# Kernel optimization log

Hardware: AMD Instinct MI355X
Metric: run time of the kernel (lower is better)

## Reference

```python
import jax, jax.numpy as jnp
import numpy as np

# dims (see shape_source)
N = 20000      # spots / graph nodes
G = 3000       # genes
NF = 256       # NFeature = CrossAttention dim
D_IN = 256     # dims_spot[0]
HID = 64       # dims_spot[1]
OUT = 16       # dims_spot[2]
H = 3          # GATv2 heads
E1 = 640000
E2 = 320000
SLOPE = 0.2    # leaky relu negative slope (GATv2 + CrossAttention alpha)


def _gat_params(key, din, hid, heads):
    k = jax.random.split(key, 3)
    s = 1.0 / np.sqrt(din)
    Wl = jax.random.normal(k[0], (din, heads * hid), jnp.float32) * s
    Wr = jax.random.normal(k[1], (din, heads * hid), jnp.float32) * s
    att = jax.random.normal(k[2], (heads, hid), jnp.float32) * s
    bl = jnp.zeros((heads * hid,), jnp.float32)
    br = jnp.zeros((heads * hid,), jnp.float32)
    b = jnp.zeros((hid,), jnp.float32)
    return Wl, bl, Wr, br, att, b


def setup_inputs() -> dict:
    key = jax.random.key(0)
    ks = jax.random.split(key, 16)
    inp = {
        "gene_freq_mtx": jax.random.normal(ks[0], (NF, G), jnp.float32),
        "gene_eigvecs_T": jax.random.normal(ks[1], (G, N), jnp.float32) / np.sqrt(G),
        "spot_freq_mtx": jax.random.normal(ks[2], (N, D_IN), jnp.float32),
        "spot_eigvecs_T": jax.random.normal(ks[3], (D_IN, NF), jnp.float32) / np.sqrt(D_IN),
        "spotnet": jax.random.randint(ks[4], (2, E1), 0, N, jnp.int32),
        "spotnet_cluster": jax.random.randint(ks[5], (2, E2), 0, N, jnp.int32),
    }
    for name, din, kk in [("c1", D_IN, ks[6]), ("c1p", D_IN, ks[7]), ("c3", OUT, ks[8]), ("c3p", OUT, ks[9])]:
        Wl, bl, Wr, br, att, b = _gat_params(kk, din, HID, H)
        inp[name + "_Wl"] = Wl; inp[name + "_bl"] = bl
        inp[name + "_Wr"] = Wr; inp[name + "_br"] = br
        inp[name + "_att"] = att; inp[name + "_b"] = b
    inp["W2"] = jax.random.normal(ks[10], (2 * HID, OUT), jnp.float32) / np.sqrt(2 * HID)
    inp["b2"] = jnp.zeros((OUT,), jnp.float32)
    inp["W4"] = jax.random.normal(ks[11], (2 * HID, D_IN), jnp.float32) / np.sqrt(2 * HID)
    inp["b4"] = jnp.zeros((D_IN,), jnp.float32)
    inp["a1"] = jax.random.normal(ks[12], (2 * NF, 1), jnp.float32) * 0.05
    inp["a2"] = jax.random.normal(ks[13], (2 * NF, 1), jnp.float32) * 0.05
    return inp


def gatv2(x, edge_index, Wl, bl, Wr, br, att, b, n):
    """PyG GATv2Conv, concat=False (head mean), add_self_loops=False, eval mode."""
    heads, c = att.shape
    src, dst = edge_index[0], edge_index[1]
    xl = (x @ Wl + bl).reshape(-1, heads, c)   # source transform [N,H,C]
    xr = (x @ Wr + br).reshape(-1, heads, c)   # target transform [N,H,C]
    m = jax.nn.leaky_relu(xl[src] + xr[dst], SLOPE)          # [E,H,C]
    e = jnp.einsum('ehc,hc->eh', m, att)                      # [E,H]
    emax = jax.ops.segment_max(e, dst, num_segments=n)        # [N,H]
    emax = jnp.where(jnp.isfinite(emax), emax, 0.0)           # empty segments
    p = jnp.exp(e - emax[dst])
    denom = jax.ops.segment_sum(p, dst, num_segments=n)       # [N,H]
    alpha = p / jnp.maximum(denom, 1e-16)[dst]                # segment softmax
    out = jax.ops.segment_sum(alpha[:, :, None] * xl[src], dst, num_segments=n)
    return out.mean(axis=1) + b                                # [N,C]


def reference(gene_freq_mtx, gene_eigvecs_T, spot_freq_mtx, spot_eigvecs_T,
              c1_Wl, c1_bl, c1_Wr, c1_br, c1_att, c1_b,
              c1p_Wl, c1p_bl, c1p_Wr, c1p_br, c1p_att, c1p_b,
              W2, b2,
              c3_Wl, c3_bl, c3_Wr, c3_br, c3_att, c3_b,
              c3p_Wl, c3p_bl, c3p_Wr, c3p_br, c3p_att, c3p_b,
              W4, b4, a1, a2, spotnet, spotnet_cluster):
    n = spot_freq_mtx.shape[0]
    # GAT (cluster=True)
    h1n = gatv2(spot_freq_mtx, spotnet, c1_Wl, c1_bl, c1_Wr, c1_br, c1_att, c1_b, n)
    h1p = gatv2(spot_freq_mtx, spotnet_cluster, c1p_Wl, c1p_bl, c1p_Wr, c1p_br, c1p_att, c1p_b, n)
    h1 = jax.nn.elu(jnp.concatenate([h1n, h1p], axis=1))
    h2 = h1 @ W2 + b2                                          # emb_spot [N,OUT]
    h3n = gatv2(h2, spotnet, c3_Wl, c3_bl, c3_Wr, c3_br, c3_att, c3_b, n)
    h3p = gatv2(h2, spotnet_cluster, c3p_Wl, c3p_bl, c3p_Wr, c3p_br, c3p_att, c3p_b, n)
    h3 = jax.nn.elu(jnp.concatenate([h3n, h3p], axis=1))
    h4 = h3 @ W4 + b4                                          # mtx_res_spot [N,D_IN]
    # iGFT + clip-at-zero (== relu)
    Xg = jax.nn.relu(gene_eigvecs_T.T @ gene_freq_mtx.T)       # [N,NF]
    Xs = jax.nn.relu(h4 @ spot_eigvecs_T)                      # [N,NF]
    # CrossAttention (dropout=0.0)
    cat = jnp.concatenate([Xg, Xs], axis=1)                    # [N,2NF]
    e = jax.nn.leaky_relu(jnp.concatenate([cat @ a1, cat @ a2], axis=1), SLOPE)
    lam = jax.nn.softmax(e, axis=1)                            # [N,2]
    res = lam[:, :1] * Xg + lam[:, 1:] * Xs
    return (res, lam, h2, h4)
```

## Files before the change

### kernel.cpp

```cpp
#include <hip/hip_runtime.h>

typedef unsigned short u16;
typedef __attribute__((ext_vector_type(8))) short bf16x8;
typedef __attribute__((ext_vector_type(4))) float floatx4;

#define NSPOT 20000
#define NGENE 3000
#define E1N   640000
#define E2N   320000

#define OFF_RES 0
#define OFF_LAM 5120000
#define OFF_H2  5160000
#define OFF_H4  5480000

__device__ __forceinline__ float b2f(u16 u){
  union { unsigned int i; float f; } v; v.i = ((unsigned int)u) << 16; return v.f;
}
__device__ __forceinline__ u16 f2b(float f){
  union { float f; unsigned int i; } v; v.f = f;
  unsigned int i = v.i;
  return (u16)((i + 0x7FFFu + ((i >> 16) & 1u)) >> 16);
}
__device__ __forceinline__ void stout(void* O, size_t i, float v, int isbf){
  if (isbf) ((u16*)O)[i] = f2b(v); else ((float*)O)[i] = v;
}
__device__ __forceinline__ u16 ldu(const void* p, size_t i, int isbf){
  return isbf ? ((const u16*)p)[i] : f2b(((const float*)p)[i]);
}

__global__ void sniff_kernel(const u16* __restrict__ x, int* __restrict__ flag){
  int lane = threadIdx.x;
  u16 u = x[lane * 2];
  int e = (u >> 7) & 0xFF;
  int sane = (u == 0) || (e >= 0x60 && e <= 0xA0);
  unsigned long long b = __ballot(sane);
  if (lane == 0) flag[0] = (__popcll(b) >= 48) ? 1 : 0;
}

struct ConvSeg { const void* src; u16* dst; int n; };
struct ConvBatch { ConvSeg s[14]; };
__global__ void convbatch_kernel(ConvBatch cb, const int* __restrict__ dflag){
  ConvSeg S = cb.s[blockIdx.y];
  int i = blockIdx.x * 256 + threadIdx.x;
  if (i < S.n) S.dst[i] = ldu(S.src, i, dflag[0]);
}

__global__ void conv3_kernel(const void* __restrict__ s0, u16* __restrict__ d0, int n0,
                             const void* __restrict__ s1, u16* __restrict__ d1, int n1,
                             const void* __restrict__ s2, u16* __restrict__ d2, int n2,
                             const int* __restrict__ dflag){
  int i = blockIdx.x * 256 + threadIdx.x;
  const void* src; u16* dst; int local;
  if (i < n0){ src = s0; dst = d0; local = i; }
  else if (i < n0 + n1){ src = s1; dst = d1; local = i - n0; }
  else if (i < n0 + n1 + n2){ src = s2; dst = d2; local = i - n0 - n1; }
  else return;
  size_t b = (size_t)local * 4;
  u16 o[4];
  if (dflag[0]){
    *(uint2*)o = *(const uint2*)((const u16*)src + b);
  } else {
    float4 f = *(const float4*)((const float*)src + b);
    o[0]=f2b(f.x); o[1]=f2b(f.y); o[2]=f2b(f.z); o[3]=f2b(f.w);
  }
  *(uint2*)(dst + b) = *(uint2*)o;
}

__global__ void hist2_kernel(const int* __restrict__ dst0, int E0, int* __restrict__ cnt0,
                             const int* __restrict__ dst1, int E1, int* __restrict__ cnt1){
  const int* dst = blockIdx.y ? dst1 : dst0;
  int* cnt = blockIdx.y ? cnt1 : cnt0;
  int E = blockIdx.y ? E1 : E0;
  int e = blockIdx.x * 256 + threadIdx.x;
  if (e < E){ int d = dst[e]; if ((unsigned)d < (unsigned)NSPOT) atomicAdd(&cnt[d], 1); }
}

__global__ void scan2_kernel(const int* __restrict__ c0, int* __restrict__ o0, int* __restrict__ u0,
                             const int* __restrict__ c1, int* __restrict__ o1, int* __restrict__ u1,
                             int n){
  const int* cnt = blockIdx.x ? c1 : c0;
  int* off = blockIdx.x ? o1 : o0;
  int* cur = blockIdx.x ? u1 : u0;
  __shared__ int part[256];
  int tid = threadIdx.x;
  int chunk = (n + 255) / 256;
  int lo = tid * chunk; if (lo > n) lo = n;
  int hi = lo + chunk; if (hi > n) hi = n;
  int s = 0;
  for (int i = lo; i < hi; i++) s += cnt[i];
  part[tid] = s;
  __syncthreads();
  if (tid == 0){
    int run = 0;
    for (int i = 0; i < 256; i++){ int t = part[i]; part[i] = run; run += t; }
  }
  __syncthreads();
  int run = part[tid];
  for (int i = lo; i < hi; i++){ off[i] = run; cur[i] = run; run += cnt[i]; }
  if (hi == n) off[n] = run;
}

__global__ void scatter2_kernel(const int* __restrict__ src0, const int* __restrict__ dst0,
                                int* __restrict__ cur0, int* __restrict__ out0, int E0,
                                const int* __restrict__ src1, const int* __restrict__ dst1,
                                int* __restrict__ cur1, int* __restrict__ out1, int E1){
  const int* src = blockIdx.y ? src1 : src0;
  const int* dst = blockIdx.y ? dst1 : dst0;
  int* cur = blockIdx.y ? cur1 : cur0;
  int* out = blockIdx.y ? out1 : out0;
  int E = blockIdx.y ? E1 : E0;
  int e = blockIdx.x * 256 + threadIdx.x;
  if (e < E){
    int d = dst[e];
    if ((unsigned)d < (unsigned)NSPOT){
      int p = atomicAdd(&cur[d], 1);
      if ((unsigned)p < (unsigned)E) out[p] = src[e];
    }
  }
}

struct AsmSet {
  const void *Wl, *bl, *Wr, *br, *Wlp, *blp, *Wrp, *brp;
  u16* Wcat; u16* bcat; int Kdim;
};
__global__ void assemble2_kernel(AsmSet s0, AsmSet s1, const int* __restrict__ dflag){
  AsmSet S = blockIdx.y ? s1 : s0;
  int isbf = dflag[0];
  int idx = blockIdx.x * 256 + threadIdx.x;
  int total = S.Kdim * 768;
  if (idx < total){
    int k = idx / 768, j = idx % 768;
    int seg = j / 192, jj = j % 192;
    const void* W = (seg == 0) ? S.Wl : (seg == 1) ? S.Wr : (seg == 2) ? S.Wlp : S.Wrp;
    S.Wcat[idx] = ldu(W, (size_t)k * 192 + jj, isbf);
  }
  if (idx < 768){
    int seg = idx / 192, jj = idx % 192;
    const void* b = (seg == 0) ? S.bl : (seg == 1) ? S.br : (seg == 2) ? S.blp : S.brp;
    S.bcat[idx] = ldu(b, jj, isbf);
  }
}

template<int BMI, bool A_KM, bool B_NK, bool A_EXT, bool B_EXT, bool RELU, bool HAS_BIAS, bool C_OUT, bool C2, bool C_F32>
__global__ __launch_bounds__(256) void gemm_mfma(
    const void* __restrict__ A, const void* __restrict__ B,
    const u16* __restrict__ bias, void* __restrict__ Cp, u16* __restrict__ Cp2,
    const int* __restrict__ dflag, size_t aoff, size_t coff,
    int M, int N, int K, int kchunk, size_t cstride,
    int lda, int ldb, int ldc, int ldc2)
{
  const int isbf = dflag[0];
  constexpr int BM = 64 * BMI, BK = 32, LDA = BK + 8, LDB = BK + 8;
  __shared__ __align__(16) u16 As[BM * LDA];
  __shared__ __align__(16) u16 Bs[64 * LDB];
  const u16*   A16 = (const u16*)A + aoff;
  const float* A32 = (const float*)A + aoff;
  const u16*   B16 = (const u16*)B;
  const float* B32 = (const float*)B;
  auto ldA = [&](size_t i) -> u16 { return (!A_EXT || isbf) ? A16[i] : f2b(A32[i]); };
  auto ldB = [&](size_t i) -> u16 { return (!B_EXT || isbf) ? B16[i] : f2b(B32[i]); };

  int tid = threadIdx.x;
  int lane = tid & 63, w = tid >> 6;
  int m0 = blockIdx.y * BM, n0 = blockIdx.x * 64;
  int kbeg = (int)blockIdx.z * kchunk;
  int kend = (K < kbeg + kchunk) ? K : (kbeg + kchunk);
  floatx4 acc[BMI][4] = {};
  int quad = lane >> 4;
  int nk = (kend - kbeg + BK - 1) / BK;
  for (int kt = 0; kt < nk; kt++){
    int k0 = kbeg + kt * BK;
    if (!A_KM){
#pragma unroll
      for (int i = 0; i < BMI; i++){
        int id = tid + i * 256;
        int r = id >> 2, c = (id & 3) * 8;
        int gm = m0 + r, gk = k0 + c;
        if (gm < M && gk + 8 <= K){
          if (!A_EXT || isbf){
            *(uint4*)&As[r * LDA + c] = *(const uint4*)(A16 + (size_t)gm * lda + gk);
          } else {
            const float* p = A32 + (size_t)gm * lda + gk;
            float4 f0 = *(const float4*)p, f1 = *(const float4*)(p + 4);
            u16* d = &As[r * LDA + c];
            d[0]=f2b(f0.x); d[1]=f2b(f0.y); d[2]=f2b(f0.z); d[3]=f2b(f0.w);
            d[4]=f2b(f1.x); d[5]=f2b(f1.y); d[6]=f2b(f1.z); d[7]=f2b(f1.w);
          }
        } else {
          for (int e = 0; e < 8; e++)
            As[r * LDA + c + e] = (gm < M && gk + e < K) ? ldA((size_t)gm * lda + gk + e) : (u16)0;
        }
      }
    } else {
#pragma unroll
      for (int i = 0; i < BMI; i++){
        int id = tid + i * 256;
        int kk, rr;
        if (BMI == 2){ kk = id >> 4; rr = (id & 15) * 8; }
        else         { kk = id >> 3; rr = (id & 7) * 8; }
        int gk = k0 + kk, gm = m0 + rr;
        if (gk < K && gm + 8 <= M){
          if (!A_EXT || isbf){
            uint4 v = *(const uint4*)(A16 + (size_t)gk * lda + gm);
            const u16* pv = (const u16*)&v;
#pragma unroll
            for (int e = 0; e < 8; e++) As[(rr + e) * LDA + kk] = pv[e];
          } else {
            const float* p = A32 + (size_t)gk * lda + gm;
            float4 f0 = *(const float4*)p, f1 = *(const float4*)(p + 4);
            As[(rr+0)*LDA+kk]=f2b(f0.x); As[(rr+1)*LDA+kk]=f2b(f0.y);
            As[(rr+2)*LDA+kk]=f2b(f0.z); As[(rr+3)*LDA+kk]=f2b(f0.w);
            As[(rr+4)*LDA+kk]=f2b(f1.x); As[(rr+5)*LDA+kk]=f2b(f1.y);
            As[(rr+6)*LDA+kk]=f2b(f1.z); As[(rr+7)*LDA+kk]=f2b(f1.w);
          }
        } else {
          for (int e = 0; e < 8; e++)
            As[(rr + e) * LDA + kk] = (gk < K && gm + e < M) ? ldA((size_t)gk * lda + gm + e) : (u16)0;
        }
      }
    }
    if (B_NK){
      int r = tid >> 2, c = (tid & 3) * 8;
      int gn = n0 + r, gk = k0 + c;
      if (gn < N && gk + 8 <= K){
        if (!B_EXT || isbf){
          *(uint4*)&Bs[r * LDB + c] = *(const uint4*)(B16 + (size_t)gn * ldb + gk);
        } else {
          const float* p = B32 + (size_t)gn * ldb + gk;
          float4 f0 = *(const float4*)p, f1 = *(const float4*)(p + 4);
          u16* d = &Bs[r * LDB + c];
          d[0]=f2b(f0.x); d[1]=f2b(f0.y); d[2]=f2b(f0.z); d[3]=f2b(f0.w);
          d[4]=f2b(f1.x); d[5]=f2b(f1.y); d[6]=f2b(f1.z); d[7]=f2b(f1.w);
        }
      } else {
        for (int e = 0; e < 8; e++)
          Bs[r * LDB + c + e] = (gn < N && gk + e < K) ? ldB((size_t)gn * ldb + gk + e) : (u16)0;
      }
    } else {
      int kk = tid >> 3, nn = (tid & 7) * 8;
      int gk = k0 + kk, gn = n0 + nn;
      if (gk < K && gn + 8 <= N){
        if (!B_EXT || isbf){
          uint4 v = *(const uint4*)(B16 + (size_t)gk * ldb + gn);
          const u16* pv = (const u16*)&v;
#pragma unroll
          for (int e = 0; e < 8; e++) Bs[(nn + e) * LDB + kk] = pv[e];
        } else {
          const float* p = B32 + (size_t)gk * ldb + gn;
          float4 f0 = *(const float4*)p, f1 = *(const float4*)(p + 4);
          Bs[(nn+0)*LDB+kk]=f2b(f0.x); Bs[(nn+1)*LDB+kk]=f2b(f0.y);
          Bs[(nn+2)*LDB+kk]=f2b(f0.z); Bs[(nn+3)*LDB+kk]=f2b(f0.w);
          Bs[(nn+4)*LDB+kk]=f2b(f1.x); Bs[(nn+5)*LDB+kk]=f2b(f1.y);
          Bs[(nn+6)*LDB+kk]=f2b(f1.z); Bs[(nn+7)*LDB+kk]=f2b(f1.w);
        }
      } else {
        for (int e = 0; e < 8; e++)
          Bs[(nn + e) * LDB + kk] = (gk < K && gn + e < N) ? ldB((size_t)gk * ldb + gn + e) : (u16)0;
      }
    }
    __syncthreads();
    bf16x8 af[BMI];
#pragma unroll
    for (int mi = 0; mi < BMI; mi++)
      af[mi] = *(const bf16x8*)&As[(w * (16 * BMI) + mi * 16 + (lane & 15)) * LDA + quad * 8];
#pragma unroll
    for (int ni = 0; ni < 4; ni++){
      bf16x8 bfr = *(const bf16x8*)&Bs[(ni * 16 + (lane & 15)) * LDB + quad * 8];
#pragma unroll
      for (int mi = 0; mi < BMI; mi++)
        acc[mi][ni] = __builtin_amdgcn_mfma_f32_16x16x32_bf16(af[mi], bfr, acc[mi][ni], 0, 0, 0);
    }
    __syncthreads();
  }
#pragma unroll
  for (int mi = 0; mi < BMI; mi++)
#pragma unroll
    for (int ni = 0; ni < 4; ni++)
#pragma unroll
      for (int r = 0; r < 4; r++){
        int row = m0 + w * (16 * BMI) + mi * 16 + quad * 4 + r;
        int col = n0 + ni * 16 + (lane & 15);
        if (row < M && col < N){
          float v = acc[mi][ni][r];
          if (HAS_BIAS) v += b2f(bias[col]);
          if (RELU) v = fmaxf(v, 0.f);
          size_t ci = coff + (size_t)blockIdx.z * cstride + (size_t)row * ldc + col;
          if (C_F32) ((float*)Cp)[ci] = v;
          else if (!C_OUT) ((u16*)Cp)[ci] = f2b(v);
          else stout(Cp, ci, v, isbf);
          if (C2) Cp2[(size_t)row * ldc2 + col] = f2b(v);
        }
      }
}

__global__ __launch_bounds__(256) void redtr_kernel(const float* __restrict__ P,
                                                    u16* __restrict__ XG){
  __shared__ float tile[64 * 65];
  int s0 = blockIdx.x * 64;
  int c0 = blockIdx.y * 64;
  int t = threadIdx.x;
#pragma unroll
  for (int i = 0; i < 4; i++){
    int c = i * 16 + (t >> 4);
    int sp = (t & 15) * 4;
    int gs = s0 + sp;
    size_t base = (size_t)(c0 + c) * NSPOT + gs;
    float v0 = 0.f, v1 = 0.f, v2 = 0.f, v3 = 0.f;
    if (gs + 4 <= NSPOT){
      float4 a = *(const float4*)(P + base);
      float4 b = *(const float4*)(P + (size_t)256 * NSPOT + base);
      v0 = a.x + b.x; v1 = a.y + b.y; v2 = a.z + b.z; v3 = a.w + b.w;
    } else {
      for (int e = 0; e < 4; e++){
        if (gs + e < NSPOT){
          float x = P[base + e] + P[(size_t)256 * NSPOT + base + e];
          if (e == 0) v0 = x; else if (e == 1) v1 = x; else if (e == 2) v2 = x; else v3 = x;
        }
      }
    }
    tile[c * 65 + sp + 0] = fmaxf(v0, 0.f);
    tile[c * 65 + sp + 1] = fmaxf(v1, 0.f);
    tile[c * 65 + sp + 2] = fmaxf(v2, 0.f);
    tile[c * 65 + sp + 3] = fmaxf(v3, 0.f);
  }
  __syncthreads();
#pragma unroll
  for (int i = 0; i < 2; i++){
    int sp = i * 32 + (t >> 3);
    int cc = (t & 7) * 8;
    int gs = s0 + sp;
    if (gs < NSPOT){
      u16 o[8];
#pragma unroll
      for (int e = 0; e < 8; e++) o[e] = f2b(tile[(cc + e) * 65 + sp]);
      *(uint4*)&XG[(size_t)gs * 256 + c0 + cc] = *(uint4*)o;
    }
  }
}

struct GatSet {
  const int* off; const int* srcs; const u16* att; const u16* bias;
  int xl_off, xr_off, out_off, E;
};
__global__ __launch_bounds__(256) void gat2_kernel(
    const u16* __restrict__ Y, GatSet SA, GatSet SB,
    u16* __restrict__ aggout, int n)
{
  int half = gridDim.x >> 1;
  int selB = (int)blockIdx.x >= half;
  GatSet S = selB ? SB : SA;
  int bx = blockIdx.x - (selB ? half : 0);
  int wid = (bx * 256 + threadIdx.x) >> 6;
  int lane = threadIdx.x & 63;
  if (wid >= n) return;
  int sub = lane >> 3;
  int cbase = (lane & 7) * 8;
  const int ldY = 768;
  size_t drow = (size_t)wid * ldY;

  float xr[3][8], at[3][8];
#pragma unroll
  for (int h = 0; h < 3; h++){
    uint4 vx = *(const uint4*)(Y + drow + S.xr_off + h * 64 + cbase);
    uint4 va = *(const uint4*)(S.att + h * 64 + cbase);
    const u16* px = (const u16*)&vx;
    const u16* pa = (const u16*)&va;
#pragma unroll
    for (int j = 0; j < 8; j++){ xr[h][j] = b2f(px[j]); at[h][j] = b2f(pa[j]); }
  }

  int beg = S.off[wid], end = S.off[wid + 1];
  beg = max(0, min(beg, S.E));
  end = max(beg, min(end, S.E));

  float mh[3] = {-INFINITY, -INFINITY, -INFINITY};
  float lh[3] = {0.f, 0.f, 0.f};
  float ac[3][8] = {};

  uint4 xa[3] = {};
  int s_b = 0;
  if (beg < end){
    int e0 = beg + sub;
    int s = (e0 < end) ? S.srcs[e0] : 0;
    if ((unsigned)s >= (unsigned)NSPOT) s = 0;
    const u16* p = Y + (size_t)s * ldY + S.xl_off + cbase;
#pragma unroll
    for (int h = 0; h < 3; h++) xa[h] = *(const uint4*)(p + h * 64);
    if (beg + 8 < end){
      int e1 = beg + 8 + sub;
      int s1 = (e1 < end) ? S.srcs[e1] : 0;
      if ((unsigned)s1 >= (unsigned)NSPOT) s1 = 0;
      s_b = s1;
    }
  }

  for (int b = beg; b < end; b += 8){
    uint4 xc[3];
#pragma unroll
    for (int h = 0; h < 3; h++) xc[h] = xa[h];
    bool act = (b + sub) < end;

    if (b + 8 < end){
      const u16* p = Y + (size_t)s_b * ldY + S.xl_off + cbase;
#pragma unroll
      for (int h = 0; h < 3; h++) xa[h] = *(const uint4*)(p + h * 64);
      if (b + 16 < end){
        int e2 = b + 16 + sub;
        int s2 = (e2 < end) ? S.srcs[e2] : 0;
        if ((unsigned)s2 >= (unsigned)NSPOT) s2 = 0;
        s_b = s2;
      }
    }

    float xl[3][8];
    float t0 = 0.f, t1 = 0.f, t2 = 0.f;
    {
      const u16* p0 = (const u16*)&xc[0];
      const u16* p1 = (const u16*)&xc[1];
      const u16* p2 = (const u16*)&xc[2];
#pragma unroll
      for (int j = 0; j < 8; j++){
        float x0 = b2f(p0[j]); xl[0][j] = x0;
        float u0 = x0 + xr[0][j]; u0 = fmaxf(u0, 0.2f * u0);
        t0 = __builtin_fmaf(at[0][j], u0, t0);
        float x1 = b2f(p1[j]); xl[1][j] = x1;
        float u1 = x1 + xr[1][j]; u1 = fmaxf(u1, 0.2f * u1);
        t1 = __builtin_fmaf(at[1][j], u1, t1);
        float x2 = b2f(p2[j]); xl[2][j] = x2;
        float u2 = x2 + xr[2][j]; u2 = fmaxf(u2, 0.2f * u2);
        t2 = __builtin_fmaf(at[2][j], u2, t2);
      }
    }
#pragma unroll
    for (int d = 1; d < 8; d <<= 1){
      t0 += __shfl_xor(t0, d, 64);
      t1 += __shfl_xor(t1, d, 64);
      t2 += __shfl_xor(t2, d, 64);
    }
    if (act){
      float tt[3] = {t0, t1, t2};
#pragma unroll
      for (int h = 0; h < 3; h++){
        float nm = fmaxf(mh[h], tt[h]);
        if (nm > mh[h]){
          float sc = __expf(mh[h] - nm);
          lh[h] *= sc;
#pragma unroll
          for (int j = 0; j < 8; j++) ac[h][j] *= sc;
          mh[h] = nm;
        }
        float w = __expf(tt[h] - mh[h]);
        lh[h] += w;
#pragma unroll
        for (int j = 0; j < 8; j++) ac[h][j] = __builtin_fmaf(w, xl[h][j], ac[h][j]);
      }
    }
  }

  float o[8] = {};
#pragma unroll
  for (int h = 0; h < 3; h++){
    float gm = fmaxf(mh[h], __shfl_xor(mh[h], 8, 64));
    gm = fmaxf(gm, __shfl_xor(gm, 16, 64));
    gm = fmaxf(gm, __shfl_xor(gm, 32, 64));
    float sc = (mh[h] == -INFINITY) ? 0.f : __expf(mh[h] - gm);
    float L = lh[h] * sc;
    L += __shfl_xor(L, 8, 64);
    L += __shfl_xor(L, 16, 64);
    L += __shfl_xor(L, 32, 64);
    float inv = 1.f / fmaxf(L, 1e-16f);
#pragma unroll
    for (int j = 0; j < 8; j++){
      float a = ac[h][j] * sc;
      a += __shfl_xor(a, 8, 64);
      a += __shfl_xor(a, 16, 64);
      a += __shfl_xor(a, 32, 64);
      o[j] += a * inv;
    }
  }
  if (sub == 0){
    u16 ov[8];
#pragma unroll
    for (int j = 0; j < 8; j++){
      float v = o[j] * (1.f / 3.f) + b2f(S.bias[cbase + j]);
      v = (v > 0.f) ? v : expm1f(v);
      if (!(fabsf(v) < 1e30f)) v = 0.f;
      ov[j] = f2b(v);
    }
    *(uint4*)&aggout[(size_t)wid * 128 + S.out_off + cbase] = *(uint4*)ov;
  }
}

__global__ __launch_bounds__(256) void h2y2_kernel(
    const u16* __restrict__ AGG, const u16* __restrict__ W2, const u16* __restrict__ b2,
    const u16* __restrict__ Wcat2, const u16* __restrict__ bcat2,
    void* __restrict__ OUT, u16* __restrict__ Y2,
    const int* __restrict__ dflag, int n){
  __shared__ float w2s[128 * 16];
  __shared__ float as_[16][128];
  __shared__ float h[16][16];
  __shared__ __align__(16) u16 ws_[16 * 768];
  int isbf = dflag[0];
  int tid = threadIdx.x;
  for (int i = tid; i < 128 * 16; i += 256) w2s[i] = b2f(W2[i]);
  for (int i = tid; i < 1536; i += 256) ((uint4*)ws_)[i] = ((const uint4*)Wcat2)[i];
  int m0 = blockIdx.x * 16;
  for (int i = tid; i < 16 * 128; i += 256){
    int r = i >> 7, c = i & 127; int m = m0 + r;
    as_[r][c] = (m < n) ? b2f(AGG[(size_t)m * 128 + c]) : 0.f;
  }
  __syncthreads();
  {
    int r = tid >> 4, j = tid & 15;
    int m = m0 + r;
    float acc = b2f(b2[j]);
    for (int k = 0; k < 128; k++) acc += as_[r][k] * w2s[k * 16 + j];
    h[r][j] = acc;
    if (m < n) stout(OUT, (size_t)OFF_H2 + (size_t)m * 16 + j, acc, isbf);
  }
  __syncthreads();
  int j = tid;
  float acc[16][3];
  float bj0 = b2f(bcat2[j]), bj1 = b2f(bcat2[j + 256]), bj2 = b2f(bcat2[j + 512]);
#pragma unroll
  for (int r = 0; r < 16; r++){ acc[r][0] = bj0; acc[r][1] = bj1; acc[r][2] = bj2; }
  for (int k = 0; k < 16; k++){
    float w0 = b2f(ws_[k * 768 + j]);
    float w1 = b2f(ws_[k * 768 + j + 256]);
    float w2 = b2f(ws_[k * 768 + j + 512]);
#pragma unroll
    for (int r = 0; r < 16; r++){
      float hv = h[r][k];
      acc[r][0] += hv * w0; acc[r][1] += hv * w1; acc[r][2] += hv * w2;
    }
  }
#pragma unroll
  for (int r = 0; r < 16; r++){
    int m = m0 + r;
    if (m < n){
      size_t base = (size_t)m * 768;
      Y2[base + j] = f2b(acc[r][0]);
      Y2[base + j + 256] = f2b(acc[r][1]);
      Y2[base + j + 512] = f2b(acc[r][2]);
    }
  }
}

__global__ __launch_bounds__(256) void cross_attn_kernel(
    const u16* __restrict__ XG, const u16* __restrict__ XS,
    const u16* __restrict__ a1, const u16* __restrict__ a2,
    void* __restrict__ OUT, const int* __restrict__ dflag, int n){
  int wid = (blockIdx.x * 256 + threadIdx.x) >> 6;
  int lane = threadIdx.x & 63;
  if (wid >= n) return;
  int isbf = dflag[0];
  int c0 = lane * 4;
  size_t base = (size_t)wid * 256 + c0;
  float g[4], s[4];
#pragma unroll
  for (int e = 0; e < 4; e++){ g[e] = b2f(XG[base + e]); s[e] = b2f(XS[base + e]); }
  float p1 = 0.f, p2 = 0.f;
#pragma unroll
  for (int e = 0; e < 4; e++){
    p1 += g[e] * b2f(a1[c0 + e]) + s[e] * b2f(a1[256 + c0 + e]);
    p2 += g[e] * b2f(a2[c0 + e]) + s[e] * b2f(a2[256 + c0 + e]);
  }
#pragma unroll
  for (int d = 32; d > 0; d >>= 1){
    p1 += __shfl_xor(p1, d, 64);
    p2 += __shfl_xor(p2, d, 64);
  }
  float e1 = (p1 > 0.f) ? p1 : 0.2f * p1;
  float e2 = (p2 > 0.f) ? p2 : 0.2f * p2;
  float mx = fmaxf(e1, e2);
  float w1 = __expf(e1 - mx), w2 = __expf(e2 - mx);
  float inv = 1.f / (w1 + w2);
  float l0 = w1 * inv, l1 = w2 * inv;
#pragma unroll
  for (int e = 0; e < 4; e++)
    stout(OUT, (size_t)OFF_RES + base + e, l0 * g[e] + l1 * s[e], isbf);
  if (lane == 0){
    stout(OUT, (size_t)OFF_LAM + (size_t)wid * 2,     l0, isbf);
    stout(OUT, (size_t)OFF_LAM + (size_t)wid * 2 + 1, l1, isbf);
  }
}

extern "C" void kernel_launch(void* const* d_in, const int* in_sizes, int n_in,
                              void* d_out, int out_size, void* d_ws, size_t ws_size,
                              hipStream_t stream) {
  const void* gene_freq = d_in[0];
  const void* gene_eig  = d_in[1];
  const void* spot_freq = d_in[2];
  const void* spot_eig  = d_in[3];
  const int* net1 = (const int*)d_in[4];
  const int* net2 = (const int*)d_in[5];
  const void *c1_Wl=d_in[6],  *c1_bl=d_in[7],  *c1_Wr=d_in[8],  *c1_br=d_in[9],  *c1_att=d_in[10], *c1_b=d_in[11];
  const void *c1p_Wl=d_in[12],*c1p_bl=d_in[13],*c1p_Wr=d_in[14],*c1p_br=d_in[15],*c1p_att=d_in[16],*c1p_b=d_in[17];
  const void *c3_Wl=d_in[18], *c3_bl=d_in[19], *c3_Wr=d_in[20], *c3_br=d_in[21], *c3_att=d_in[22], *c3_b=d_in[23];
  const void *c3p_Wl=d_in[24],*c3p_bl=d_in[25],*c3p_Wr=d_in[26],*c3p_br=d_in[27],*c3p_att=d_in[28],*c3p_b=d_in[29];
  const void *W2=d_in[30], *b2=d_in[31], *W4=d_in[32], *b4=d_in[33], *a1=d_in[34], *a2=d_in[35];

  char* p0 = (char*)d_ws;
  char* p = p0;
  auto carve = [&](size_t bytes) -> char* {
    char* r = p; p += (bytes + 255) & ~(size_t)255; return r;
  };
  int*   flag  = (int*) carve(256);
  int*   cnt1  = (int*) carve((NSPOT + 2) * 4);
  int*   off1  = (int*) carve((NSPOT + 2) * 4);
  int*   cur1  = (int*) carve((NSPOT + 2) * 4);
  int*   srcs1 = (int*) carve((size_t)E1N * 4);
  int*   cnt2  = (int*) carve((NSPOT + 2) * 4);
  int*   off2  = (int*) carve((NSPOT + 2) * 4);
  int*   cur2  = (int*) carve((NSPOT + 2) * 4);
  int*   srcs2 = (int*) carve((size_t)E2N * 4);
  u16*   Wcat1 = (u16*) carve(256 * 768 * 2);
  u16*   bcat1 = (u16*) carve(2048);
  u16*   Wcat2 = (u16*) carve(16 * 768 * 2);
  u16*   bcat2 = (u16*) carve(2048);
  u16*   attc1  = (u16*)carve(192 * 2);
  u16*   attc1p = (u16*)carve(192 * 2);
  u16*   attc3  = (u16*)carve(192 * 2);
  u16*   attc3p = (u16*)carve(192 * 2);
  u16*   bc1  = (u16*)carve(64 * 2);
  u16*   bc1p = (u16*)carve(64 * 2);
  u16*   bc3  = (u16*)carve(64 * 2);
  u16*   bc3p = (u16*)carve(64 * 2);
  u16*   W2c  = (u16*)carve(2048 * 2);
  u16*   b2c  = (u16*)carve(16 * 2);
  u16*   W4c  = (u16*)carve(32768 * 2);
  u16*   b4c  = (u16*)carve(256 * 2);
  u16*   a1c  = (u16*)carve(512 * 2);
  u16*   a2c  = (u16*)carve(512 * 2);
  u16*   GF16 = (u16*) carve((size_t)256 * 3000 * 2);
  u16*   SE16 = (u16*) carve((size_t)256 * 256 * 2);
  u16*   SF16 = (u16*) carve((size_t)NSPOT * 256 * 2);
  u16*   H4B  = (u16*) carve((size_t)NSPOT * 256 * 2);
  u16*   AGG  = (u16*) carve((size_t)NSPOT * 128 * 2);
  u16*   XG   = (u16*) carve((size_t)NSPOT * 256 * 2);
  char*  R    = carve((size_t)2 * 256 * NSPOT * 4);
  float* Pbuf = (float*)R;
  u16*   Y    = (u16*)R;
  u16*   XS   = (u16*)(R + (size_t)NSPOT * 768 * 2);

  sniff_kernel<<<1, 64, 0, stream>>>((const u16*)spot_freq, flag);
  hipMemsetAsync(cnt1, 0, NSPOT * 4, stream);
  hipMemsetAsync(cnt2, 0, NSPOT * 4, stream);
  hist2_kernel<<<dim3((E1N + 255) / 256, 2), 256, 0, stream>>>(
      net1 + E1N, E1N, cnt1, net2 + E2N, E2N, cnt2);
  scan2_kernel<<<2, 256, 0, stream>>>(cnt1, off1, cur1, cnt2, off2, cur2, NSPOT);
  scatter2_kernel<<<dim3((E1N + 255) / 256, 2), 256, 0, stream>>>(
      net1, net1 + E1N, cur1, srcs1, E1N, net2, net2 + E2N, cur2, srcs2, E2N);

  ConvBatch cb;
  cb.s[0]  = {c1_att,  attc1,  192}; cb.s[1]  = {c1p_att, attc1p, 192};
  cb.s[2]  = {c3_att,  attc3,  192}; cb.s[3]  = {c3p_att, attc3p, 192};
  cb.s[4]  = {c1_b, bc1, 64}; cb.s[5]  = {c1p_b, bc1p, 64};
  cb.s[6]  = {c3_b, bc3, 64}; cb.s[7]  = {c3p_b, bc3p, 64};
  cb.s[8]  = {W2, W2c, 2048}; cb.s[9]  = {b2, b2c, 16};
  cb.s[10] = {W4, W4c, 32768}; cb.s[11] = {b4, b4c, 256};
  cb.s[12] = {a1, a1c, 512}; cb.s[13] = {a2, a2c, 512};
  convbatch_kernel<<<dim3(128, 14), 256, 0, stream>>>(cb, flag);

  {
    int n0 = 256 * 3000 / 4, n1 = 256 * 256 / 4, n2 = NSPOT * 256 / 4;
    int tot = n0 + n1 + n2;
    conv3_kernel<<<(tot + 255) / 256, 256, 0, stream>>>(
        gene_freq, GF16, n0, spot_eig, SE16, n1, spot_freq, SF16, n2, flag);
  }

  AsmSet as0 = {c1_Wl, c1_bl, c1_Wr, c1_br, c1p_Wl, c1p_bl, c1p_Wr, c1p_br, Wcat1, bcat1, 256};
  AsmSet as1 = {c3_Wl, c3_bl, c3_Wr, c3_br, c3p_Wl, c3p_bl, c3p_Wr, c3p_br, Wcat2, bcat2, 16};
  assemble2_kernel<<<dim3((256 * 768 + 255) / 256, 2), 256, 0, stream>>>(as0, as1, flag);

  GatSet g1a = {off1, srcs1, attc1,  bc1,  0,   192, 0,  E1N};
  GatSet g1b = {off2, srcs2, attc1p, bc1p, 384, 576, 64, E2N};
  GatSet g3a = {off1, srcs1, attc3,  bc3,  0,   192, 0,  E1N};
  GatSet g3b = {off2, srcs2, attc3p, bc3p, 384, 576, 64, E2N};

  gemm_mfma<2, false, false, false, true, false, false, false, false, true>
      <<<dim3(313, 2, 2), 256, 0, stream>>>(
      GF16, gene_eig, nullptr, Pbuf, nullptr, flag, 0, 0,
      256, NSPOT, NGENE, 1504, (size_t)256 * NSPOT, NGENE, NSPOT, NSPOT, 0);
  redtr_kernel<<<dim3(313, 4), 256, 0, stream>>>(Pbuf, XG);

  gemm_mfma<2, false, false, false, false, false, true, false, false, false>
      <<<dim3(12, 157), 256, 0, stream>>>(
      SF16, Wcat1, bcat1, Y, nullptr, flag, 0, 0,
      NSPOT, 768, 256, 256, 0, 256, 768, 768, 0);
  gat2_kernel<<<10000, 256, 0, stream>>>(Y, g1a, g1b, AGG, NSPOT);
  h2y2_kernel<<<1250, 256, 0, stream>>>(AGG, W2c, b2c, Wcat2, bcat2, d_out, Y, flag, NSPOT);
  gat2_kernel<<<10000, 256, 0, stream>>>(Y, g3a, g3b, AGG, NSPOT);
  gemm_mfma<1, false, false, false, false, false, true, true, true, false>
      <<<dim3(4, 313), 256, 0, stream>>>(
      AGG, W4c, b4c, d_out, H4B, flag, 0, OFF_H4,
      NSPOT, 256, 128, 128, 0, 128, 256, 256, 256);
  gemm_mfma<1, false, false, false, false, true, false, false, false, false>
      <<<dim3(4, 313), 256, 0, stream>>>(
      H4B, SE16, nullptr, XS, nullptr, flag, 0, 0,
      NSPOT, 256, 256, 256, 0, 256, 256, 256, 0);
  cross_attn_kernel<<<5000, 256, 0, stream>>>(XG, XS, a1c, a2c, d_out, flag, NSPOT);

  (void)in_sizes; (void)n_in; (void)out_size; (void)ws_size;
}
```

Before: 1.024 ms.

## Replace split-K gene GEMM and reduce-transpose with a fused XG kernel

Swaps the split-K gemm (written as fp32 partials) plus the separate reduce/transpose/relu kernel for one kernel that computes the whole 256xN XG output per 64-spot block. Each block stages gene_freq chunks in LDS and reads gene_eigvecs columns straight from global memory, applying relu and writing bf16 rows directly. This drops the fp32 partial buffer round-trip and one launch. The cost is lower parallelism: 313 blocks with 64 accumulator registers per thread, each block reloading all of GF and doing strided scalar global loads of GE.

```diff
diff --git a/kernel.cpp b/kernel.cpp
--- a/kernel.cpp
+++ b/kernel.cpp
@@ -142,13 +142,79 @@
   }
 }
 
-template<int BMI, bool A_KM, bool B_NK, bool A_EXT, bool B_EXT, bool RELU, bool HAS_BIAS, bool C_OUT, bool C2, bool C_F32>
+__global__ __launch_bounds__(256) void xg_kernel(
+    const u16* __restrict__ GF,
+    const void* __restrict__ GE,
+    u16* __restrict__ XG,
+    const int* __restrict__ dflag)
+{
+  constexpr int KC = 128;
+  constexpr int LDA = KC + 8;
+  __shared__ __align__(16) u16 As[256 * LDA];
+  const int isbf = dflag[0];
+  const float* GE32 = (const float*)GE;
+  const u16*   GE16 = (const u16*)GE;
+  int tid = threadIdx.x;
+  int lane = tid & 63, w = tid >> 6;
+  int quad = lane >> 4, c16 = lane & 15;
+  int n = blockIdx.x * 64 + w * 16 + c16;
+  int nc = min(n, NSPOT - 1);
+  floatx4 acc[16] = {};
+  const int NCH = (NGENE + KC - 1) / KC;
+  for (int ch = 0; ch < NCH; ch++){
+    int k0 = ch * KC;
+    {
+      const u16* src = GF + (size_t)tid * NGENE + k0;
+      u16* dst = &As[tid * LDA];
+#pragma unroll
+      for (int i = 0; i < KC / 8; i++){
+        if (k0 + i * 8 + 8 <= NGENE){
+          *(uint4*)(dst + i * 8) = *(const uint4*)(src + i * 8);
+        } else {
+          for (int e = 0; e < 8; e++)
+            dst[i * 8 + e] = (k0 + i * 8 + e < NGENE) ? src[i * 8 + e] : (u16)0;
+        }
+      }
+    }
+    __syncthreads();
+#pragma unroll
+    for (int s = 0; s < KC / 32; s++){
+      u16 bfr[8];
+#pragma unroll
+      for (int j = 0; j < 8; j++){
+        int k = k0 + s * 32 + quad * 8 + j;
+        int kcl = min(k, NGENE - 1);
+        float bv = isbf ? b2f(GE16[(size_t)kcl * NSPOT + nc])
+                        : GE32[(size_t)kcl * NSPOT + nc];
+        bfr[j] = f2b(bv);
+      }
+      bf16x8 bv8 = *(bf16x8*)bfr;
+#pragma unroll
+      for (int mt = 0; mt < 16; mt++){
+        bf16x8 av = *(const bf16x8*)&As[(mt * 16 + c16) * LDA + s * 32 + quad * 8];
+        acc[mt] = __builtin_amdgcn_mfma_f32_16x16x32_bf16(av, bv8, acc[mt], 0, 0, 0);
+      }
+    }
+    __syncthreads();
+  }
+  if (n < NSPOT){
+    u16* row = XG + (size_t)n * 256;
+#pragma unroll
+    for (int mt = 0; mt < 16; mt++){
+      u16 o[4];
+#pragma unroll
+      for (int r = 0; r < 4; r++) o[r] = f2b(fmaxf(acc[mt][r], 0.f));
+      *(uint2*)(row + mt * 16 + quad * 4) = *(uint2*)o;
+    }
+  }
+}
+
+template<int BMI, bool A_KM, bool B_NK, bool A_EXT, bool B_EXT, bool RELU, bool HAS_BIAS, bool C_OUT, bool C2>
 __global__ __launch_bounds__(256) void gemm_mfma(
     const void* __restrict__ A, const void* __restrict__ B,
     const u16* __restrict__ bias, void* __restrict__ Cp, u16* __restrict__ Cp2,
     const int* __restrict__ dflag, size_t aoff, size_t coff,
-    int M, int N, int K, int kchunk, size_t cstride,
-    int lda, int ldb, int ldc, int ldc2)
+    int M, int N, int K, int lda, int ldb, int ldc, int ldc2)
 {
   const int isbf = dflag[0];
   constexpr int BM = 64 * BMI, BK = 32, LDA = BK + 8, LDB = BK + 8;
@@ -164,13 +230,11 @@
   int tid = threadIdx.x;
   int lane = tid & 63, w = tid >> 6;
   int m0 = blockIdx.y * BM, n0 = blockIdx.x * 64;
-  int kbeg = (int)blockIdx.z * kchunk;
-  int kend = (K < kbeg + kchunk) ? K : (kbeg + kchunk);
   floatx4 acc[BMI][4] = {};
   int quad = lane >> 4;
-  int nk = (kend - kbeg + BK - 1) / BK;
+  int nk = (K + BK - 1) / BK;
   for (int kt = 0; kt < nk; kt++){
-    int k0 = kbeg + kt * BK;
+    int k0 = kt * BK;
     if (!A_KM){
 #pragma unroll
       for (int i = 0; i < BMI; i++){
@@ -285,58 +349,12 @@
           float v = acc[mi][ni][r];
           if (HAS_BIAS) v += b2f(bias[col]);
           if (RELU) v = fmaxf(v, 0.f);
-          size_t ci = coff + (size_t)blockIdx.z * cstride + (size_t)row * ldc + col;
-          if (C_F32) ((float*)Cp)[ci] = v;
-          else if (!C_OUT) ((u16*)Cp)[ci] = f2b(v);
+          size_t ci = coff + (size_t)row * ldc + col;
+          if (!C_OUT) ((u16*)Cp)[ci] = f2b(v);
           else stout(Cp, ci, v, isbf);
           if (C2) Cp2[(size_t)row * ldc2 + col] = f2b(v);
         }
       }
-}
-
-__global__ __launch_bounds__(256) void redtr_kernel(const float* __restrict__ P,
-                                                    u16* __restrict__ XG){
-  __shared__ float tile[64 * 65];
-  int s0 = blockIdx.x * 64;
-  int c0 = blockIdx.y * 64;
-  int t = threadIdx.x;
-#pragma unroll
-  for (int i = 0; i < 4; i++){
-    int c = i * 16 + (t >> 4);
-    int sp = (t & 15) * 4;
-    int gs = s0 + sp;
-    size_t base = (size_t)(c0 + c) * NSPOT + gs;
-    float v0 = 0.f, v1 = 0.f, v2 = 0.f, v3 = 0.f;
-    if (gs + 4 <= NSPOT){
-      float4 a = *(const float4*)(P + base);
-      float4 b = *(const float4*)(P + (size_t)256 * NSPOT + base);
-      v0 = a.x + b.x; v1 = a.y + b.y; v2 = a.z + b.z; v3 = a.w + b.w;
-    } else {
-      for (int e = 0; e < 4; e++){
-        if (gs + e < NSPOT){
-          float x = P[base + e] + P[(size_t)256 * NSPOT + base + e];
-          if (e == 0) v0 = x; else if (e == 1) v1 = x; else if (e == 2) v2 = x; else v3 = x;
-        }
-      }
-    }
-    tile[c * 65 + sp + 0] = fmaxf(v0, 0.f);
-    tile[c * 65 + sp + 1] = fmaxf(v1, 0.f);
-    tile[c * 65 + sp + 2] = fmaxf(v2, 0.f);
-    tile[c * 65 + sp + 3] = fmaxf(v3, 0.f);
-  }
-  __syncthreads();
-#pragma unroll
-  for (int i = 0; i < 2; i++){
-    int sp = i * 32 + (t >> 3);
-    int cc = (t & 7) * 8;
-    int gs = s0 + sp;
-    if (gs < NSPOT){
-      u16 o[8];
-#pragma unroll
-      for (int e = 0; e < 8; e++) o[e] = f2b(tile[(cc + e) * 65 + sp]);
-      *(uint4*)&XG[(size_t)gs * 256 + c0 + cc] = *(uint4*)o;
-    }
-  }
 }
 
 struct GatSet {
@@ -640,7 +658,6 @@
   u16*   AGG  = (u16*) carve((size_t)NSPOT * 128 * 2);
   u16*   XG   = (u16*) carve((size_t)NSPOT * 256 * 2);
   char*  R    = carve((size_t)2 * 256 * NSPOT * 4);
-  float* Pbuf = (float*)R;
   u16*   Y    = (u16*)R;
   u16*   XS   = (u16*)(R + (size_t)NSPOT * 768 * 2);
 
@@ -679,27 +696,23 @@
   GatSet g3a = {off1, srcs1, attc3,  bc3,  0,   192, 0,  E1N};
   GatSet g3b = {off2, srcs2, attc3p, bc3p, 384, 576, 64, E2N};
 
-  gemm_mfma<2, false, false, false, true, false, false, false, false, true>
-      <<<dim3(313, 2, 2), 256, 0, stream>>>(
-      GF16, gene_eig, nullptr, Pbuf, nullptr, flag, 0, 0,
-      256, NSPOT, NGENE, 1504, (size_t)256 * NSPOT, NGENE, NSPOT, NSPOT, 0);
-  redtr_kernel<<<dim3(313, 4), 256, 0, stream>>>(Pbuf, XG);
-
-  gemm_mfma<2, false, false, false, false, false, true, false, false, false>
+  xg_kernel<<<313, 256, 0, stream>>>(GF16, gene_eig, XG, flag);
+
+  gemm_mfma<2, false, false, false, false, false, true, false, false>
       <<<dim3(12, 157), 256, 0, stream>>>(
       SF16, Wcat1, bcat1, Y, nullptr, flag, 0, 0,
-      NSPOT, 768, 256, 256, 0, 256, 768, 768, 0);
+      NSPOT, 768, 256, 256, 768, 768, 0);
   gat2_kernel<<<10000, 256, 0, stream>>>(Y, g1a, g1b, AGG, NSPOT);
   h2y2_kernel<<<1250, 256, 0, stream>>>(AGG, W2c, b2c, Wcat2, bcat2, d_out, Y, flag, NSPOT);
   gat2_kernel<<<10000, 256, 0, stream>>>(Y, g3a, g3b, AGG, NSPOT);
-  gemm_mfma<1, false, false, false, false, false, true, true, true, false>
+  gemm_mfma<1, false, false, false, false, false, true, true, true>
       <<<dim3(4, 313), 256, 0, stream>>>(
       AGG, W4c, b4c, d_out, H4B, flag, 0, OFF_H4,
-      NSPOT, 256, 128, 128, 0, 128, 256, 256, 256);
-  gemm_mfma<1, false, false, false, false, true, false, false, false, false>
+      NSPOT, 256, 128, 128, 256, 256, 256);
+  gemm_mfma<1, false, false, false, false, true, false, false, false>
       <<<dim3(4, 313), 256, 0, stream>>>(
       H4B, SE16, nullptr, XS, nullptr, flag, 0, 0,
-      NSPOT, 256, 256, 256, 0, 256, 256, 256, 0);
+      NSPOT, 256, 256, 256, 256, 256, 0);
   cross_attn_kernel<<<5000, 256, 0, stream>>>(XG, XS, a1c, a2c, d_out, flag, NSPOT);
 
   (void)in_sizes; (void)n_in; (void)out_size; (void)ws_size;
```

Result: slower. 1.102 ms (+7.6%).

## Write gene GEMM partials transposed and split K four ways with simpler reduction

Applied to the files above, without the earlier changes.

The gene-frequency GEMM now writes its fp32 split-K partials directly in spot-major (transposed) layout using float4 stores, so the follow-up kernel becomes a plain elementwise sum, relu and bf16 convert with no shared-memory transpose. The GEMM tile grows to BM=256 (covering all 256 rows in one block), and the K split goes from 2 to 4 chunks of 768. This removes the separate transpose pass and raises parallelism over K. In exchange the partial buffer doubles in size, and the reduction kernel reads four fp32 planes. The transposed float4 stores are strided by column, which may hurt write coalescing.

```diff
diff --git a/kernel.cpp b/kernel.cpp
--- a/kernel.cpp
+++ b/kernel.cpp
@@ -142,7 +142,7 @@
   }
 }
 
-template<int BMI, bool A_KM, bool B_NK, bool A_EXT, bool B_EXT, bool RELU, bool HAS_BIAS, bool C_OUT, bool C2, bool C_F32>
+template<int BMI, bool A_KM, bool B_NK, bool A_EXT, bool B_EXT, bool RELU, bool HAS_BIAS, bool C_OUT, bool C2, bool C_F32TR>
 __global__ __launch_bounds__(256) void gemm_mfma(
     const void* __restrict__ A, const void* __restrict__ B,
     const u16* __restrict__ bias, void* __restrict__ Cp, u16* __restrict__ Cp2,
@@ -273,6 +273,23 @@
     }
     __syncthreads();
   }
+  if (C_F32TR){
+#pragma unroll
+    for (int mi = 0; mi < BMI; mi++)
+#pragma unroll
+      for (int ni = 0; ni < 4; ni++){
+        int rowb = m0 + w * (16 * BMI) + mi * 16 + quad * 4;
+        int col = n0 + ni * 16 + (lane & 15);
+        if (col < N && rowb + 4 <= M){
+          float4 o;
+          o.x = acc[mi][ni][0]; o.y = acc[mi][ni][1];
+          o.z = acc[mi][ni][2]; o.w = acc[mi][ni][3];
+          *(float4*)((float*)Cp + coff + (size_t)blockIdx.z * cstride
+                     + (size_t)col * ldc + rowb) = o;
+        }
+      }
+    return;
+  }
 #pragma unroll
   for (int mi = 0; mi < BMI; mi++)
 #pragma unroll
@@ -285,58 +302,29 @@
           float v = acc[mi][ni][r];
           if (HAS_BIAS) v += b2f(bias[col]);
           if (RELU) v = fmaxf(v, 0.f);
-          size_t ci = coff + (size_t)blockIdx.z * cstride + (size_t)row * ldc + col;
-          if (C_F32) ((float*)Cp)[ci] = v;
-          else if (!C_OUT) ((u16*)Cp)[ci] = f2b(v);
+          size_t ci = coff + (size_t)row * ldc + col;
+          if (!C_OUT) ((u16*)Cp)[ci] = f2b(v);
           else stout(Cp, ci, v, isbf);
           if (C2) Cp2[(size_t)row * ldc2 + col] = f2b(v);
         }
       }
 }
 
-__global__ __launch_bounds__(256) void redtr_kernel(const float* __restrict__ P,
+__global__ __launch_bounds__(256) void xgred_kernel(const float* __restrict__ P,
                                                     u16* __restrict__ XG){
-  __shared__ float tile[64 * 65];
-  int s0 = blockIdx.x * 64;
-  int c0 = blockIdx.y * 64;
-  int t = threadIdx.x;
-#pragma unroll
-  for (int i = 0; i < 4; i++){
-    int c = i * 16 + (t >> 4);
-    int sp = (t & 15) * 4;
-    int gs = s0 + sp;
-    size_t base = (size_t)(c0 + c) * NSPOT + gs;
-    float v0 = 0.f, v1 = 0.f, v2 = 0.f, v3 = 0.f;
-    if (gs + 4 <= NSPOT){
-      float4 a = *(const float4*)(P + base);
-      float4 b = *(const float4*)(P + (size_t)256 * NSPOT + base);
-      v0 = a.x + b.x; v1 = a.y + b.y; v2 = a.z + b.z; v3 = a.w + b.w;
-    } else {
-      for (int e = 0; e < 4; e++){
-        if (gs + e < NSPOT){
-          float x = P[base + e] + P[(size_t)256 * NSPOT + base + e];
-          if (e == 0) v0 = x; else if (e == 1) v1 = x; else if (e == 2) v2 = x; else v3 = x;
-        }
-      }
-    }
-    tile[c * 65 + sp + 0] = fmaxf(v0, 0.f);
-    tile[c * 65 + sp + 1] = fmaxf(v1, 0.f);
-    tile[c * 65 + sp + 2] = fmaxf(v2, 0.f);
-    tile[c * 65 + sp + 3] = fmaxf(v3, 0.f);
-  }
-  __syncthreads();
-#pragma unroll
-  for (int i = 0; i < 2; i++){
-    int sp = i * 32 + (t >> 3);
-    int cc = (t & 7) * 8;
-    int gs = s0 + sp;
-    if (gs < NSPOT){
-      u16 o[8];
-#pragma unroll
-      for (int e = 0; e < 8; e++) o[e] = f2b(tile[(cc + e) * 65 + sp]);
-      *(uint4*)&XG[(size_t)gs * 256 + c0 + cc] = *(uint4*)o;
-    }
-  }
+  size_t i = ((size_t)blockIdx.x * 256 + threadIdx.x) * 4;
+  const size_t ZS = (size_t)NSPOT * 256;
+  if (i >= ZS) return;
+  float4 a = *(const float4*)(P + i);
+  float4 b = *(const float4*)(P + ZS + i);
+  float4 c = *(const float4*)(P + 2 * ZS + i);
+  float4 d = *(const float4*)(P + 3 * ZS + i);
+  u16 o[4];
+  o[0] = f2b(fmaxf(a.x + b.x + c.x + d.x, 0.f));
+  o[1] = f2b(fmaxf(a.y + b.y + c.y + d.y, 0.f));
+  o[2] = f2b(fmaxf(a.z + b.z + c.z + d.z, 0.f));
+  o[3] = f2b(fmaxf(a.w + b.w + c.w + d.w, 0.f));
+  *(uint2*)(XG + i) = *(uint2*)o;
 }
 
 struct GatSet {
@@ -639,7 +627,7 @@
   u16*   H4B  = (u16*) carve((size_t)NSPOT * 256 * 2);
   u16*   AGG  = (u16*) carve((size_t)NSPOT * 128 * 2);
   u16*   XG   = (u16*) carve((size_t)NSPOT * 256 * 2);
-  char*  R    = carve((size_t)2 * 256 * NSPOT * 4);
+  char*  R    = carve((size_t)4 * NSPOT * 256 * 4);
   float* Pbuf = (float*)R;
   u16*   Y    = (u16*)R;
   u16*   XS   = (u16*)(R + (size_t)NSPOT * 768 * 2);
@@ -679,11 +667,11 @@
   GatSet g3a = {off1, srcs1, attc3,  bc3,  0,   192, 0,  E1N};
   GatSet g3b = {off2, srcs2, attc3p, bc3p, 384, 576, 64, E2N};
 
-  gemm_mfma<2, false, false, false, true, false, false, false, false, true>
-      <<<dim3(313, 2, 2), 256, 0, stream>>>(
+  gemm_mfma<4, false, false, false, true, false, false, false, false, true>
+      <<<dim3(313, 1, 4), 256, 0, stream>>>(
       GF16, gene_eig, nullptr, Pbuf, nullptr, flag, 0, 0,
-      256, NSPOT, NGENE, 1504, (size_t)256 * NSPOT, NGENE, NSPOT, NSPOT, 0);
-  redtr_kernel<<<dim3(313, 4), 256, 0, stream>>>(Pbuf, XG);
+      256, NSPOT, NGENE, 768, (size_t)NSPOT * 256, NGENE, NSPOT, 256, 0);
+  xgred_kernel<<<5000, 256, 0, stream>>>(Pbuf, XG);
 
   gemm_mfma<2, false, false, false, false, false, true, false, false, false>
       <<<dim3(12, 157), 256, 0, stream>>>(
```

New measurement: 1.045 ms. +2.1%, slower.

## Split gene GEMM K four ways, rotate LDS transpose stores, separate f32 epilogue

Applied to the files above, without the earlier changes.

Raises the split-K factor of the gene-eigvec GEMM from 2 to 4 (chunk 768). This doubles the number of workgroups and improves occupancy across the CUs, and the reduce-transpose kernel now sums four partial buffers. The transposed B-tile LDS stores are rotated per thread to spread bank accesses and cut LDS bank conflicts. The f32 output path also gets its own early-return epilogue. In exchange, the scratch buffer doubles and the reduce kernel reads twice as much partial data.

```diff
diff --git a/kernel.cpp b/kernel.cpp
--- a/kernel.cpp
+++ b/kernel.cpp
@@ -240,19 +240,22 @@
     } else {
       int kk = tid >> 3, nn = (tid & 7) * 8;
       int gk = k0 + kk, gn = n0 + nn;
+      int rot = tid & 7;
       if (gk < K && gn + 8 <= N){
+        u16 tv[8];
         if (!B_EXT || isbf){
           uint4 v = *(const uint4*)(B16 + (size_t)gk * ldb + gn);
-          const u16* pv = (const u16*)&v;
-#pragma unroll
-          for (int e = 0; e < 8; e++) Bs[(nn + e) * LDB + kk] = pv[e];
+          *(uint4*)tv = v;
         } else {
           const float* p = B32 + (size_t)gk * ldb + gn;
           float4 f0 = *(const float4*)p, f1 = *(const float4*)(p + 4);
-          Bs[(nn+0)*LDB+kk]=f2b(f0.x); Bs[(nn+1)*LDB+kk]=f2b(f0.y);
-          Bs[(nn+2)*LDB+kk]=f2b(f0.z); Bs[(nn+3)*LDB+kk]=f2b(f0.w);
-          Bs[(nn+4)*LDB+kk]=f2b(f1.x); Bs[(nn+5)*LDB+kk]=f2b(f1.y);
-          Bs[(nn+6)*LDB+kk]=f2b(f1.z); Bs[(nn+7)*LDB+kk]=f2b(f1.w);
+          tv[0]=f2b(f0.x); tv[1]=f2b(f0.y); tv[2]=f2b(f0.z); tv[3]=f2b(f0.w);
+          tv[4]=f2b(f1.x); tv[5]=f2b(f1.y); tv[6]=f2b(f1.z); tv[7]=f2b(f1.w);
+        }
+#pragma unroll
+        for (int ee = 0; ee < 8; ee++){
+          int e = (ee + rot) & 7;
+          Bs[(nn + e) * LDB + kk] = tv[e];
         }
       } else {
         for (int e = 0; e < 8; e++)
@@ -272,6 +275,21 @@
         acc[mi][ni] = __builtin_amdgcn_mfma_f32_16x16x32_bf16(af[mi], bfr, acc[mi][ni], 0, 0, 0);
     }
     __syncthreads();
+  }
+  if (C_F32){
+#pragma unroll
+    for (int mi = 0; mi < BMI; mi++)
+#pragma unroll
+      for (int ni = 0; ni < 4; ni++)
+#pragma unroll
+        for (int r = 0; r < 4; r++){
+          int row = m0 + w * (16 * BMI) + mi * 16 + quad * 4 + r;
+          int col = n0 + ni * 16 + (lane & 15);
+          if (row < M && col < N)
+            ((float*)Cp)[coff + (size_t)blockIdx.z * cstride + (size_t)row * ldc + col]
+                = acc[mi][ni][r];
+        }
+    return;
   }
 #pragma unroll
   for (int mi = 0; mi < BMI; mi++)
@@ -285,9 +303,8 @@
           float v = acc[mi][ni][r];
           if (HAS_BIAS) v += b2f(bias[col]);
           if (RELU) v = fmaxf(v, 0.f);
-          size_t ci = coff + (size_t)blockIdx.z * cstride + (size_t)row * ldc + col;
-          if (C_F32) ((float*)Cp)[ci] = v;
-          else if (!C_OUT) ((u16*)Cp)[ci] = f2b(v);
+          size_t ci = coff + (size_t)row * ldc + col;
+          if (!C_OUT) ((u16*)Cp)[ci] = f2b(v);
           else stout(Cp, ci, v, isbf);
           if (C2) Cp2[(size_t)row * ldc2 + col] = f2b(v);
         }
@@ -300,6 +317,7 @@
   int s0 = blockIdx.x * 64;
   int c0 = blockIdx.y * 64;
   int t = threadIdx.x;
+  const size_t ZS = (size_t)256 * NSPOT;
 #pragma unroll
   for (int i = 0; i < 4; i++){
     int c = i * 16 + (t >> 4);
@@ -309,12 +327,15 @@
     float v0 = 0.f, v1 = 0.f, v2 = 0.f, v3 = 0.f;
     if (gs + 4 <= NSPOT){
       float4 a = *(const float4*)(P + base);
-      float4 b = *(const float4*)(P + (size_t)256 * NSPOT + base);
-      v0 = a.x + b.x; v1 = a.y + b.y; v2 = a.z + b.z; v3 = a.w + b.w;
+      float4 b = *(const float4*)(P + ZS + base);
+      float4 cc = *(const float4*)(P + 2 * ZS + base);
+      float4 d = *(const float4*)(P + 3 * ZS + base);
+      v0 = a.x + b.x + cc.x + d.x; v1 = a.y + b.y + cc.y + d.y;
+      v2 = a.z + b.z + cc.z + d.z; v3 = a.w + b.w + cc.w + d.w;
     } else {
       for (int e = 0; e < 4; e++){
         if (gs + e < NSPOT){
-          float x = P[base + e] + P[(size_t)256 * NSPOT + base + e];
+          float x = P[base + e] + P[ZS + base + e] + P[2 * ZS + base + e] + P[3 * ZS + base + e];
           if (e == 0) v0 = x; else if (e == 1) v1 = x; else if (e == 2) v2 = x; else v3 = x;
         }
       }
@@ -639,7 +660,7 @@
   u16*   H4B  = (u16*) carve((size_t)NSPOT * 256 * 2);
   u16*   AGG  = (u16*) carve((size_t)NSPOT * 128 * 2);
   u16*   XG   = (u16*) carve((size_t)NSPOT * 256 * 2);
-  char*  R    = carve((size_t)2 * 256 * NSPOT * 4);
+  char*  R    = carve((size_t)4 * 256 * NSPOT * 4);
   float* Pbuf = (float*)R;
   u16*   Y    = (u16*)R;
   u16*   XS   = (u16*)(R + (size_t)NSPOT * 768 * 2);
@@ -680,9 +701,9 @@
   GatSet g3b = {off2, srcs2, attc3p, bc3p, 384, 576, 64, E2N};
 
   gemm_mfma<2, false, false, false, true, false, false, false, false, true>
-      <<<dim3(313, 2, 2), 256, 0, stream>>>(
+      <<<dim3(313, 2, 4), 256, 0, stream>>>(
       GF16, gene_eig, nullptr, Pbuf, nullptr, flag, 0, 0,
-      256, NSPOT, NGENE, 1504, (size_t)256 * NSPOT, NGENE, NSPOT, NSPOT, 0);
+      256, NSPOT, NGENE, 768, (size_t)256 * NSPOT, NGENE, NSPOT, NSPOT, 0);
   redtr_kernel<<<dim3(313, 4), 256, 0, stream>>>(Pbuf, XG);
 
   gemm_mfma<2, false, false, false, false, false, true, false, false, false>
```

Measured after the change: 1.030 ms. About the same (+0.6%).
